# Optimization experiments

Measured on AMD Instinct MI355X. Metric: run time of the kernel, lower is better.

## Reference

```python
import jax, jax.numpy as jnp
import numpy as np

NUM_LABELS = 512
NUM_DEMOG = 4
N = 65536
D = 512


def setup_inputs() -> dict:
    key = jax.random.key(0)
    k1, k2, k3 = jax.random.split(key, 3)
    feats = jax.random.normal(k1, (N, D), dtype=jnp.float32)
    labels = jax.random.randint(k2, (N,), 0, NUM_LABELS, dtype=jnp.int64)
    demog_labels = jax.random.randint(k3, (N,), 0, NUM_DEMOG, dtype=jnp.int64)
    return {"feats": feats, "labels": labels, "demog_labels": demog_labels}


def reference(feats, labels, demog_labels):
    # Group id = (demog, label) pair -> flat segment id.
    G = NUM_DEMOG * NUM_LABELS
    seg = (demog_labels * NUM_LABELS + labels).astype(jnp.int32)  # [N]

    ones = jnp.ones((feats.shape[0],), dtype=feats.dtype)
    cnt = jax.ops.segment_sum(ones, seg, num_segments=G)          # [G]
    sums = jax.ops.segment_sum(feats, seg, num_segments=G)        # [G, D]
    safe_cnt = jnp.maximum(cnt, 1.0)
    mu = sums / safe_cnt[:, None]                                 # per-group mean

    # Per-sample squared distance to its group mean (== diagonal of the
    # centered Gram matrix in the original, without the O(n^2) matmul).
    d = feats - mu[seg]                                           # [N, D]
    sq = jnp.sum(d * d, axis=1)                                   # [N]

    grp_mean_dist = jax.ops.segment_sum(sq, seg, num_segments=G) / safe_cnt  # [G]

    present = (cnt > 0).astype(feats.dtype).reshape(NUM_DEMOG, NUM_LABELS)
    gm = grp_mean_dist.reshape(NUM_DEMOG, NUM_LABELS)
    # Mean over present (demog, subject) groups within each demog.
    intra = jnp.sum(gm * present, axis=1) / jnp.maximum(jnp.sum(present, axis=1), 1.0)  # [NUM_DEMOG]

    mu_intra = jnp.mean(intra)
    loss = jnp.mean(jnp.abs(intra - mu_intra))
    return loss
```

## Files before the change

kernel.cpp:

```cpp
#include <hip/hip_runtime.h>

#define NN 65536
#define DD 512
#define NUM_LABELS 512
#define NUM_DEMOG 4
#define GG (NUM_DEMOG * NUM_LABELS)
#define CAP 128

__global__ void k_hist(const int* __restrict__ labels,
                       const int* __restrict__ demog,
                       int* __restrict__ cnt,
                       int* __restrict__ order) {
    int i = blockIdx.x * blockDim.x + threadIdx.x;
    if (i >= NN) return;
    int seg = demog[i] * NUM_LABELS + labels[i];
    int pos = atomicAdd(&cnt[seg], 1);
    if (pos < CAP) order[seg * CAP + pos] = i;
}

__global__ __launch_bounds__(256, 2)
void k_group(const float* __restrict__ feats,
             const int* __restrict__ cnt,
             const int* __restrict__ order,
             float* __restrict__ gmArr) {
    int g = blockIdx.x;
    int t = threadIdx.x;
    int col = t & 127;
    int rp  = t >> 7;

    __shared__ int sidx[CAP];
    int oi = (t < CAP) ? order[g * CAP + t] : 0;
    int c = cnt[g];
    if (c > CAP) c = CAP;
    if (t < CAP) sidx[t] = oi;
    __syncthreads();

    const float4* fv = (const float4*)feats;
    float4 acc = make_float4(0.f, 0.f, 0.f, 0.f);
    float ssq = 0.f;

    int j = rp;
    for (; j + 14 < c; j += 16) {
        int i0 = sidx[j],      i1 = sidx[j + 2],  i2 = sidx[j + 4],  i3 = sidx[j + 6];
        int i4 = sidx[j + 8],  i5 = sidx[j + 10], i6 = sidx[j + 12], i7 = sidx[j + 14];
        float4 v0 = fv[(size_t)i0 * (DD / 4) + col];
        float4 v1 = fv[(size_t)i1 * (DD / 4) + col];
        float4 v2 = fv[(size_t)i2 * (DD / 4) + col];
        float4 v3 = fv[(size_t)i3 * (DD / 4) + col];
        float4 v4 = fv[(size_t)i4 * (DD / 4) + col];
        float4 v5 = fv[(size_t)i5 * (DD / 4) + col];
        float4 v6 = fv[(size_t)i6 * (DD / 4) + col];
        float4 v7 = fv[(size_t)i7 * (DD / 4) + col];
        acc.x += v0.x + v1.x + v2.x + v3.x + v4.x + v5.x + v6.x + v7.x;
        acc.y += v0.y + v1.y + v2.y + v3.y + v4.y + v5.y + v6.y + v7.y;
        acc.z += v0.z + v1.z + v2.z + v3.z + v4.z + v5.z + v6.z + v7.z;
        acc.w += v0.w + v1.w + v2.w + v3.w + v4.w + v5.w + v6.w + v7.w;
        ssq += v0.x * v0.x + v0.y * v0.y + v0.z * v0.z + v0.w * v0.w;
        ssq += v1.x * v1.x + v1.y * v1.y + v1.z * v1.z + v1.w * v1.w;
        ssq += v2.x * v2.x + v2.y * v2.y + v2.z * v2.z + v2.w * v2.w;
        ssq += v3.x * v3.x + v3.y * v3.y + v3.z * v3.z + v3.w * v3.w;
        ssq += v4.x * v4.x + v4.y * v4.y + v4.z * v4.z + v4.w * v4.w;
        ssq += v5.x * v5.x + v5.y * v5.y + v5.z * v5.z + v5.w * v5.w;
        ssq += v6.x * v6.x + v6.y * v6.y + v6.z * v6.z + v6.w * v6.w;
        ssq += v7.x * v7.x + v7.y * v7.y + v7.z * v7.z + v7.w * v7.w;
    }
    for (; j + 6 < c; j += 8) {
        int i0 = sidx[j], i1 = sidx[j + 2], i2 = sidx[j + 4], i3 = sidx[j + 6];
        float4 v0 = fv[(size_t)i0 * (DD / 4) + col];
        float4 v1 = fv[(size_t)i1 * (DD / 4) + col];
        float4 v2 = fv[(size_t)i2 * (DD / 4) + col];
        float4 v3 = fv[(size_t)i3 * (DD / 4) + col];
        acc.x += v0.x + v1.x + v2.x + v3.x;
        acc.y += v0.y + v1.y + v2.y + v3.y;
        acc.z += v0.z + v1.z + v2.z + v3.z;
        acc.w += v0.w + v1.w + v2.w + v3.w;
        ssq += v0.x * v0.x + v0.y * v0.y + v0.z * v0.z + v0.w * v0.w;
        ssq += v1.x * v1.x + v1.y * v1.y + v1.z * v1.z + v1.w * v1.w;
        ssq += v2.x * v2.x + v2.y * v2.y + v2.z * v2.z + v2.w * v2.w;
        ssq += v3.x * v3.x + v3.y * v3.y + v3.z * v3.z + v3.w * v3.w;
    }
    for (; j < c; j += 2) {
        float4 v = fv[(size_t)sidx[j] * (DD / 4) + col];
        acc.x += v.x; acc.y += v.y; acc.z += v.z; acc.w += v.w;
        ssq += v.x * v.x + v.y * v.y + v.z * v.z + v.w * v.w;
    }

    __shared__ float4 accbuf[128];
    if (rp == 1) accbuf[col] = acc;
    __syncthreads();
    float n2p = 0.f;
    if (rp == 0) {
        float4 o = accbuf[col];
        float x = acc.x + o.x, y = acc.y + o.y, z = acc.z + o.z, w = acc.w + o.w;
        n2p = x * x + y * y + z * z + w * w;
    }

    for (int off = 32; off > 0; off >>= 1) {
        ssq += __shfl_down(ssq, off);
        n2p += __shfl_down(n2p, off);
    }
    __shared__ float red[8];
    if ((t & 63) == 0) {
        int wid = t >> 6;
        red[wid * 2]     = ssq;
        red[wid * 2 + 1] = n2p;
    }
    __syncthreads();
    if (t == 0) {
        float gm = 0.f;
        if (c > 0) {
            float S  = red[0] + red[2] + red[4] + red[6];
            float N2 = red[1] + red[3] + red[5] + red[7];
            gm = (S - N2 / (float)c) / (float)c;
        }
        gmArr[g] = gm;
    }
}

__global__ __launch_bounds__(256)
void k_final(const int* __restrict__ cnt,
             const float* __restrict__ gmArr,
             float* __restrict__ out) {
    int t = threadIdx.x;
    int w = t >> 6;
    int lane = t & 63;
    __shared__ float intra[NUM_DEMOG];

    float s = 0.f;
    float p = 0.f;
    for (int l = lane; l < NUM_LABELS; l += 64) {
        int g = w * NUM_LABELS + l;
        if (cnt[g] > 0) { s += gmArr[g]; p += 1.f; }
    }
    for (int off = 32; off > 0; off >>= 1) {
        s += __shfl_down(s, off);
        p += __shfl_down(p, off);
    }
    if (lane == 0) intra[w] = s / fmaxf(p, 1.f);
    __syncthreads();
    if (t == 0) {
        float m = 0.f;
        for (int d = 0; d < NUM_DEMOG; ++d) m += intra[d];
        m *= (1.f / NUM_DEMOG);
        float l = 0.f;
        for (int d = 0; d < NUM_DEMOG; ++d) l += fabsf(intra[d] - m);
        out[0] = l * (1.f / NUM_DEMOG);
    }
}

extern "C" void kernel_launch(void* const* d_in, const int* in_sizes, int n_in,
                              void* d_out, int out_size, void* d_ws, size_t ws_size,
                              hipStream_t stream) {
    const float* feats = (const float*)d_in[0];
    const int* labels  = (const int*)d_in[1];
    const int* demog   = (const int*)d_in[2];
    float* out = (float*)d_out;

    int*   cnt   = (int*)d_ws;
    float* gmArr = (float*)(cnt + GG);
    int*   order = (int*)(gmArr + GG);

    hipMemsetAsync(d_ws, 0, GG * sizeof(int), stream);

    k_hist<<<NN / 256, 256, 0, stream>>>(labels, demog, cnt, order);
    k_group<<<GG, 256, 0, stream>>>(feats, cnt, order, gmArr);
    k_final<<<1, 256, 0, stream>>>(cnt, gmArr, out);
}
```

Measured before the change: 211.9 us.

## Pack eight groups per 1024-thread block and read indices directly with prefetch

k_group now handles eight groups per 1024-thread block, one 128-thread slice per group, each slice walking all of its group's rows, instead of two row-halves per group in a 256-thread block. This removes the shared-memory index staging, the cross-half accumulator exchange and one barrier. Indices are read from global memory as int4 vectors with one-step prefetch. k_hist moves to 512-thread blocks. The trade-off is fewer blocks and longer per-thread serial loops for each group, with fewer loads in flight per group.

```diff
diff --git a/kernel.cpp b/kernel.cpp
--- a/kernel.cpp
+++ b/kernel.cpp
@@ -6,111 +6,97 @@
 #define NUM_DEMOG 4
 #define GG (NUM_DEMOG * NUM_LABELS)
 #define CAP 128
+#define SUBS 8
+#define KG_BLOCKS (GG / SUBS)
 
-__global__ void k_hist(const int* __restrict__ labels,
-                       const int* __restrict__ demog,
-                       int* __restrict__ cnt,
-                       int* __restrict__ order) {
-    int i = blockIdx.x * blockDim.x + threadIdx.x;
-    if (i >= NN) return;
+__global__ __launch_bounds__(512)
+void k_hist(const int* __restrict__ labels,
+            const int* __restrict__ demog,
+            int* __restrict__ cnt,
+            int* __restrict__ order) {
+    int i = blockIdx.x * 512 + threadIdx.x;
     int seg = demog[i] * NUM_LABELS + labels[i];
     int pos = atomicAdd(&cnt[seg], 1);
     if (pos < CAP) order[seg * CAP + pos] = i;
 }
 
-__global__ __launch_bounds__(256, 2)
+__global__ __launch_bounds__(1024, 4)
 void k_group(const float* __restrict__ feats,
              const int* __restrict__ cnt,
              const int* __restrict__ order,
              float* __restrict__ gmArr) {
-    int g = blockIdx.x;
     int t = threadIdx.x;
+    int s = t >> 7;
     int col = t & 127;
-    int rp  = t >> 7;
+    int g = blockIdx.x * SUBS + s;
 
-    __shared__ int sidx[CAP];
-    int oi = (t < CAP) ? order[g * CAP + t] : 0;
     int c = cnt[g];
     if (c > CAP) c = CAP;
-    if (t < CAP) sidx[t] = oi;
-    __syncthreads();
 
     const float4* fv = (const float4*)feats;
+    const int* ob = order + g * CAP;
+
     float4 acc = make_float4(0.f, 0.f, 0.f, 0.f);
     float ssq = 0.f;
 
-    int j = rp;
-    for (; j + 14 < c; j += 16) {
-        int i0 = sidx[j],      i1 = sidx[j + 2],  i2 = sidx[j + 4],  i3 = sidx[j + 6];
-        int i4 = sidx[j + 8],  i5 = sidx[j + 10], i6 = sidx[j + 12], i7 = sidx[j + 14];
-        float4 v0 = fv[(size_t)i0 * (DD / 4) + col];
-        float4 v1 = fv[(size_t)i1 * (DD / 4) + col];
-        float4 v2 = fv[(size_t)i2 * (DD / 4) + col];
-        float4 v3 = fv[(size_t)i3 * (DD / 4) + col];
-        float4 v4 = fv[(size_t)i4 * (DD / 4) + col];
-        float4 v5 = fv[(size_t)i5 * (DD / 4) + col];
-        float4 v6 = fv[(size_t)i6 * (DD / 4) + col];
-        float4 v7 = fv[(size_t)i7 * (DD / 4) + col];
-        acc.x += v0.x + v1.x + v2.x + v3.x + v4.x + v5.x + v6.x + v7.x;
-        acc.y += v0.y + v1.y + v2.y + v3.y + v4.y + v5.y + v6.y + v7.y;
-        acc.z += v0.z + v1.z + v2.z + v3.z + v4.z + v5.z + v6.z + v7.z;
-        acc.w += v0.w + v1.w + v2.w + v3.w + v4.w + v5.w + v6.w + v7.w;
-        ssq += v0.x * v0.x + v0.y * v0.y + v0.z * v0.z + v0.w * v0.w;
-        ssq += v1.x * v1.x + v1.y * v1.y + v1.z * v1.z + v1.w * v1.w;
-        ssq += v2.x * v2.x + v2.y * v2.y + v2.z * v2.z + v2.w * v2.w;
-        ssq += v3.x * v3.x + v3.y * v3.y + v3.z * v3.z + v3.w * v3.w;
-        ssq += v4.x * v4.x + v4.y * v4.y + v4.z * v4.z + v4.w * v4.w;
-        ssq += v5.x * v5.x + v5.y * v5.y + v5.z * v5.z + v5.w * v5.w;
-        ssq += v6.x * v6.x + v6.y * v6.y + v6.z * v6.z + v6.w * v6.w;
-        ssq += v7.x * v7.x + v7.y * v7.y + v7.z * v7.z + v7.w * v7.w;
+    int j = 0;
+    if (j + 7 < c) {
+        int4 ia = *(const int4*)(ob + 0);
+        int4 ib = *(const int4*)(ob + 4);
+        for (; j + 7 < c; j += 8) {
+            int4 na = ia, nb = ib;
+            if (j + 15 < c) {
+                na = *(const int4*)(ob + j + 8);
+                nb = *(const int4*)(ob + j + 12);
+            }
+            float4 v0 = fv[(size_t)ia.x * (DD / 4) + col];
+            float4 v1 = fv[(size_t)ia.y * (DD / 4) + col];
+            float4 v2 = fv[(size_t)ia.z * (DD / 4) + col];
+            float4 v3 = fv[(size_t)ia.w * (DD / 4) + col];
+            float4 v4 = fv[(size_t)ib.x * (DD / 4) + col];
+            float4 v5 = fv[(size_t)ib.y * (DD / 4) + col];
+            float4 v6 = fv[(size_t)ib.z * (DD / 4) + col];
+            float4 v7 = fv[(size_t)ib.w * (DD / 4) + col];
+            acc.x += v0.x + v1.x + v2.x + v3.x + v4.x + v5.x + v6.x + v7.x;
+            acc.y += v0.y + v1.y + v2.y + v3.y + v4.y + v5.y + v6.y + v7.y;
+            acc.z += v0.z + v1.z + v2.z + v3.z + v4.z + v5.z + v6.z + v7.z;
+            acc.w += v0.w + v1.w + v2.w + v3.w + v4.w + v5.w + v6.w + v7.w;
+            ssq += v0.x * v0.x + v0.y * v0.y + v0.z * v0.z + v0.w * v0.w;
+            ssq += v1.x * v1.x + v1.y * v1.y + v1.z * v1.z + v1.w * v1.w;
+            ssq += v2.x * v2.x + v2.y * v2.y + v2.z * v2.z + v2.w * v2.w;
+            ssq += v3.x * v3.x + v3.y * v3.y + v3.z * v3.z + v3.w * v3.w;
+            ssq += v4.x * v4.x + v4.y * v4.y + v4.z * v4.z + v4.w * v4.w;
+            ssq += v5.x * v5.x + v5.y * v5.y + v5.z * v5.z + v5.w * v5.w;
+            ssq += v6.x * v6.x + v6.y * v6.y + v6.z * v6.z + v6.w * v6.w;
+            ssq += v7.x * v7.x + v7.y * v7.y + v7.z * v7.z + v7.w * v7.w;
+            ia = na; ib = nb;
+        }
     }
-    for (; j + 6 < c; j += 8) {
-        int i0 = sidx[j], i1 = sidx[j + 2], i2 = sidx[j + 4], i3 = sidx[j + 6];
-        float4 v0 = fv[(size_t)i0 * (DD / 4) + col];
-        float4 v1 = fv[(size_t)i1 * (DD / 4) + col];
-        float4 v2 = fv[(size_t)i2 * (DD / 4) + col];
-        float4 v3 = fv[(size_t)i3 * (DD / 4) + col];
-        acc.x += v0.x + v1.x + v2.x + v3.x;
-        acc.y += v0.y + v1.y + v2.y + v3.y;
-        acc.z += v0.z + v1.z + v2.z + v3.z;
-        acc.w += v0.w + v1.w + v2.w + v3.w;
-        ssq += v0.x * v0.x + v0.y * v0.y + v0.z * v0.z + v0.w * v0.w;
-        ssq += v1.x * v1.x + v1.y * v1.y + v1.z * v1.z + v1.w * v1.w;
-        ssq += v2.x * v2.x + v2.y * v2.y + v2.z * v2.z + v2.w * v2.w;
-        ssq += v3.x * v3.x + v3.y * v3.y + v3.z * v3.z + v3.w * v3.w;
-    }
-    for (; j < c; j += 2) {
-        float4 v = fv[(size_t)sidx[j] * (DD / 4) + col];
+    for (; j < c; ++j) {
+        int idx = ob[j];
+        float4 v = fv[(size_t)idx * (DD / 4) + col];
         acc.x += v.x; acc.y += v.y; acc.z += v.z; acc.w += v.w;
         ssq += v.x * v.x + v.y * v.y + v.z * v.z + v.w * v.w;
     }
 
-    __shared__ float4 accbuf[128];
-    if (rp == 1) accbuf[col] = acc;
-    __syncthreads();
-    float n2p = 0.f;
-    if (rp == 0) {
-        float4 o = accbuf[col];
-        float x = acc.x + o.x, y = acc.y + o.y, z = acc.z + o.z, w = acc.w + o.w;
-        n2p = x * x + y * y + z * z + w * w;
-    }
+    float n2p = acc.x * acc.x + acc.y * acc.y + acc.z * acc.z + acc.w * acc.w;
 
     for (int off = 32; off > 0; off >>= 1) {
         ssq += __shfl_down(ssq, off);
         n2p += __shfl_down(n2p, off);
     }
-    __shared__ float red[8];
+    __shared__ float red[SUBS][2][2];
+    int w = (t >> 6) & 1;
     if ((t & 63) == 0) {
-        int wid = t >> 6;
-        red[wid * 2]     = ssq;
-        red[wid * 2 + 1] = n2p;
+        red[s][w][0] = ssq;
+        red[s][w][1] = n2p;
     }
     __syncthreads();
-    if (t == 0) {
+    if (col == 0) {
         float gm = 0.f;
         if (c > 0) {
-            float S  = red[0] + red[2] + red[4] + red[6];
-            float N2 = red[1] + red[3] + red[5] + red[7];
+            float S  = red[s][0][0] + red[s][1][0];
+            float N2 = red[s][0][1] + red[s][1][1];
             gm = (S - N2 / (float)c) / (float)c;
         }
         gmArr[g] = gm;
@@ -162,7 +148,7 @@
 
     hipMemsetAsync(d_ws, 0, GG * sizeof(int), stream);
 
-    k_hist<<<NN / 256, 256, 0, stream>>>(labels, demog, cnt, order);
-    k_group<<<GG, 256, 0, stream>>>(feats, cnt, order, gmArr);
+    k_hist<<<NN / 512, 512, 0, stream>>>(labels, demog, cnt, order);
+    k_group<<<KG_BLOCKS, 1024, 0, stream>>>(feats, cnt, order, gmArr);
     k_final<<<1, 256, 0, stream>>>(cnt, gmArr, out);
 }
```

New measurement: 214.3 us. Within noise of the previous version (+1.2%).
